# Performance work log

Measured on AMD Instinct MI355X. Metric: run time of the kernel, lower is better.

## Reference

```python
import jax, jax.numpy as jnp
import numpy as np

N_NODES = 50000
N_EDGES = 800000
D_FEAT = 128
UNITS = 128


def setup_inputs() -> dict:
    key = jax.random.key(0)
    k1, k2, k3, k4 = jax.random.split(key, 4)
    x = jax.random.normal(k1, (N_NODES, D_FEAT), dtype=jnp.float32)
    source = jax.random.randint(k2, (N_EDGES,), 0, N_NODES, dtype=jnp.int32)
    target = jax.random.randint(k3, (N_EDGES,), 0, N_NODES, dtype=jnp.int32)
    W = jax.random.normal(k4, (D_FEAT, UNITS), dtype=jnp.float32) * (1.0 / np.sqrt(D_FEAT))
    b = jnp.zeros((UNITS,), dtype=jnp.float32)
    return {"x": x, "source": source, "target": target, "W": W, "b": b}


def _degree(idx, n_nodes):
    # in/out degree = segment-sum of unit edge weights; clamp to >= 1 (no self loops)
    deg = jnp.zeros((n_nodes,), dtype=jnp.float32).at[idx].add(1.0)
    return jnp.maximum(deg, 1.0)


def reference(x, source, target, W, b):
    n = x.shape[0]
    # degree_normalization == "in_out": sender scale from out-degree, receiver from in-degree
    sender_scale = jax.lax.rsqrt(_degree(source, n))[:, None]      # [N, 1]
    receiver_scale = jax.lax.rsqrt(_degree(target, n))[:, None]    # [N, 1]
    normalized = sender_scale * x                                  # [N, D]
    source_bcast = normalized[source]                              # [E, D] gather
    pooled = jax.ops.segment_sum(source_bcast, target, num_segments=n)  # [N, D] scatter-add
    pooled = receiver_scale * pooled
    # Dense(units, activation='relu', use_bias=True)
    return jax.nn.relu(pooled @ W + b)
```

## Files before the change

kernel.cpp:

```cpp
#include <hip/hip_runtime.h>
#include <hip/hip_bf16.h>

#define N_FEAT 128
#define EPT 8
#define CHUNK 2048
#define BSHIFT 8
#define MAXRANGE 256
#define CAP 8192
#define LSTR 66

typedef short bf16x8 __attribute__((ext_vector_type(8)));
typedef float f32x4  __attribute__((ext_vector_type(4)));

__device__ __forceinline__ unsigned short f2bf_rtne(float f) {
    unsigned u = __float_as_uint(f);
    u += 0x7fffu + ((u >> 16) & 1u);
    return (unsigned short)(u >> 16);
}
__device__ __forceinline__ float bf2f(unsigned short h) {
    return __uint_as_float((unsigned)h << 16);
}

__global__ __launch_bounds__(256) void scatter_kernel(const int* __restrict__ source,
                                                      const int* __restrict__ target,
                                                      int* __restrict__ curT,
                                                      int* __restrict__ curS,
                                                      unsigned int* __restrict__ pairsT,
                                                      unsigned char* __restrict__ srcB,
                                                      const float* __restrict__ W,
                                                      unsigned short* __restrict__ Whi,
                                                      unsigned short* __restrict__ Wlo,
                                                      int E, int NB, int NBLK) {
    __shared__ unsigned int   lds_pairs[CHUNK];
    __shared__ unsigned short lds_sp[CHUNK];
    __shared__ int ct[MAXRANGE], cs[MAXRANGE];
    __shared__ int st[MAXRANGE], ss[MAXRANGE];
    __shared__ int gt[MAXRANGE], gs[MAXRANGE];
    int tid = threadIdx.x, b = blockIdx.x;

    if (b >= NBLK) {
        int idx = (b - NBLK) * 256 + tid;
        int lane = idx & 63;
        int ks = (idx >> 6) & 3;
        int ct2 = idx >> 8;
        int n  = ct2 * 16 + (lane & 15);
        int k0 = ks * 32 + (lane >> 4) * 8;
        unsigned short h[8], l[8];
        #pragma unroll
        for (int j = 0; j < 8; ++j) {
            float w = W[(k0 + j) * N_FEAT + n];
            unsigned short hh = f2bf_rtne(w);
            h[j] = hh;
            l[j] = f2bf_rtne(w - bf2f(hh));
        }
        size_t off = (size_t)idx * 8;
        *(ushort4*)(Whi + off)     = make_ushort4(h[0], h[1], h[2], h[3]);
        *(ushort4*)(Whi + off + 4) = make_ushort4(h[4], h[5], h[6], h[7]);
        *(ushort4*)(Wlo + off)     = make_ushort4(l[0], l[1], l[2], l[3]);
        *(ushort4*)(Wlo + off + 4) = make_ushort4(l[4], l[5], l[6], l[7]);
        return;
    }

    int base = b * CHUNK;
    int cnt = E - base; if (cnt > CHUNK) cnt = CHUNK;

    int rs[EPT], rt[EPT];
    ct[tid] = 0; cs[tid] = 0;
    __syncthreads();
    #pragma unroll
    for (int j = 0; j < EPT; ++j) {
        int e = base + j * 256 + tid;
        if (e < E) {
            int s = source[e], t = target[e];
            rs[j] = s; rt[j] = t;
            atomicAdd(&ct[t >> BSHIFT], 1);
            atomicAdd(&cs[s >> BSHIFT], 1);
        }
    }
    __syncthreads();
    int vt = ct[tid], vs = cs[tid];
    st[tid] = vt; ss[tid] = vs;
    __syncthreads();
    #pragma unroll
    for (int off = 1; off < 256; off <<= 1) {
        int t1 = (tid >= off) ? st[tid - off] : 0;
        int t2 = (tid >= off) ? ss[tid - off] : 0;
        __syncthreads();
        st[tid] += t1; ss[tid] += t2;
        __syncthreads();
    }
    int et = st[tid] - vt, es = ss[tid] - vs;
    int gT = 0, gS = 0;
    if (tid < NB) {
        if (vt) gT = atomicAdd(&curT[tid], vt);
        if (vs) gS = atomicAdd(&curS[tid], vs);
    }
    __syncthreads();
    st[tid] = et; ss[tid] = es;
    ct[tid] = et; cs[tid] = es;
    gt[tid] = gT; gs[tid] = gS;
    __syncthreads();
    #pragma unroll
    for (int j = 0; j < EPT; ++j) {
        int e = base + j * 256 + tid;
        if (e < E) {
            int s = rs[j], t = rt[j];
            int k = t >> BSHIFT;
            int p = atomicAdd(&ct[k], 1);
            lds_pairs[p] = (unsigned)s | ((unsigned)t << 16);
            int k2 = s >> BSHIFT;
            int p2 = atomicAdd(&cs[k2], 1);
            lds_sp[p2] = (unsigned short)s;
        }
    }
    __syncthreads();
    for (int i = tid; i < cnt; i += 256) {
        unsigned w = lds_pairs[i];
        int k = w >> 24;
        pairsT[(size_t)k * CAP + gt[k] + (i - st[k])] = w;
        unsigned short sp = lds_sp[i];
        int k2 = sp >> 8;
        srcB[(size_t)k2 * CAP + gs[k2] + (i - ss[k2])] = (unsigned char)sp;
    }
}

__global__ __launch_bounds__(256) void prep_kernel(const unsigned char* __restrict__ srcB,
                                                   const unsigned int* __restrict__ pairsT,
                                                   const int* __restrict__ curT,
                                                   const int* __restrict__ curS,
                                                   float* __restrict__ so,
                                                   int2* __restrict__ offs,
                                                   int* __restrict__ elist,
                                                   float* __restrict__ ri,
                                                   int N, int NB) {
    __shared__ int hist[MAXRANGE];
    __shared__ int sb[MAXRANGE];
    __shared__ int excl[MAXRANGE];
    __shared__ int cur[MAXRANGE];
    int tid = threadIdx.x, b = blockIdx.x;

    if (b < NB) {
        hist[tid] = 0;
        __syncthreads();
        int cnt = curS[b];
        size_t base = (size_t)b * CAP;
        for (int i = tid; i < cnt; i += 256)
            atomicAdd(&hist[srcB[base + i]], 1);
        __syncthreads();
        int node = (b << BSHIFT) + tid;
        if (node < N) {
            int d = hist[tid]; if (d < 1) d = 1;
            so[node] = rsqrtf((float)d);
        }
    } else {
        int bb = b - NB;
        hist[tid] = 0; cur[tid] = 0;
        __syncthreads();
        int cnt = curT[bb];
        int gbase = bb * CAP;
        for (int i = tid; i < cnt; i += 256)
            atomicAdd(&hist[(pairsT[(size_t)gbase + i] >> 16) & 255], 1);
        __syncthreads();
        int deg = hist[tid];
        sb[tid] = deg;
        __syncthreads();
        #pragma unroll
        for (int off = 1; off < 256; off <<= 1) {
            int t = (tid >= off) ? sb[tid - off] : 0;
            __syncthreads();
            sb[tid] += t;
            __syncthreads();
        }
        excl[tid] = sb[tid] - deg;
        __syncthreads();
        int node = (bb << BSHIFT) + tid;
        if (node < N) {
            int st0 = gbase + excl[tid];
            offs[node] = make_int2(st0, st0 + deg);
            int d = deg; if (d < 1) d = 1;
            ri[node] = rsqrtf((float)d);
        }
        for (int i = tid; i < cnt; i += 256) {
            unsigned w = pairsT[(size_t)gbase + i];
            int tl = (w >> 16) & 255;
            int pos = atomicAdd(&cur[tl], 1);
            elist[gbase + excl[tl] + pos] = (int)(w & 0xFFFFu);
        }
    }
}

__global__ __launch_bounds__(256) void ygemm_kernel(const float* __restrict__ x,
                                                    const float* __restrict__ so,
                                                    const unsigned short* __restrict__ Whi,
                                                    const unsigned short* __restrict__ Wlo,
                                                    unsigned short* __restrict__ Y,
                                                    int N) {
    __shared__ unsigned int hi_t[16 * LSTR];
    __shared__ unsigned int lo_t[16 * LSTR];
    int tid = threadIdx.x;
    int wave = tid >> 6, lane = tid & 63;
    int quad = lane >> 4, k16 = lane & 15;
    int row0 = blockIdx.x * 16;

    for (int i = tid; i < 1024; i += 256) {
        int r = i >> 6, dw = i & 63;
        int gr = row0 + r;
        float2 v = make_float2(0.f, 0.f);
        float s = 0.f;
        if (gr < N) {
            v = ((const float2*)x)[(size_t)gr * 64 + dw];
            s = so[gr];
        }
        float v0 = s * v.x, v1 = s * v.y;
        unsigned short h0 = f2bf_rtne(v0), h1 = f2bf_rtne(v1);
        unsigned short l0 = f2bf_rtne(v0 - bf2f(h0));
        unsigned short l1 = f2bf_rtne(v1 - bf2f(h1));
        hi_t[r * LSTR + dw] = (unsigned)h0 | ((unsigned)h1 << 16);
        lo_t[r * LSTR + dw] = (unsigned)l0 | ((unsigned)l1 << 16);
    }
    __syncthreads();

    bf16x8 Ahi[4], Alo[4];
    int m = k16;
    #pragma unroll
    for (int ks = 0; ks < 4; ++ks) {
        int a = m * LSTR + ks * 16 + quad * 4;
        Ahi[ks] = *(const bf16x8*)(hi_t + a);
        Alo[ks] = *(const bf16x8*)(lo_t + a);
    }
    const bf16x8* BH = (const bf16x8*)Whi;
    const bf16x8* BL = (const bf16x8*)Wlo;
    #pragma unroll
    for (int c = 0; c < 2; ++c) {
        int ctile = wave * 2 + c;
        f32x4 acc = {0.f, 0.f, 0.f, 0.f};
        #pragma unroll
        for (int ks = 0; ks < 4; ++ks) {
            bf16x8 bh = BH[(ctile * 4 + ks) * 64 + lane];
            bf16x8 bl = BL[(ctile * 4 + ks) * 64 + lane];
            acc = __builtin_amdgcn_mfma_f32_16x16x32_bf16(Ahi[ks], bh, acc, 0, 0, 0);
            acc = __builtin_amdgcn_mfma_f32_16x16x32_bf16(Alo[ks], bh, acc, 0, 0, 0);
            acc = __builtin_amdgcn_mfma_f32_16x16x32_bf16(Ahi[ks], bl, acc, 0, 0, 0);
        }
        int colc = ctile * 16 + m;
        #pragma unroll
        for (int reg = 0; reg < 4; ++reg) {
            int gr = row0 + quad * 4 + reg;
            if (gr < N)
                Y[(size_t)gr * N_FEAT + colc] = f2bf_rtne(acc[reg]);
        }
    }
}

#define ACC8(u) { acc[0] += __uint_as_float((u).x << 16); \
                  acc[1] += __uint_as_float((u).x & 0xffff0000u); \
                  acc[2] += __uint_as_float((u).y << 16); \
                  acc[3] += __uint_as_float((u).y & 0xffff0000u); \
                  acc[4] += __uint_as_float((u).z << 16); \
                  acc[5] += __uint_as_float((u).z & 0xffff0000u); \
                  acc[6] += __uint_as_float((u).w << 16); \
                  acc[7] += __uint_as_float((u).w & 0xffff0000u); }

__global__ __launch_bounds__(128) void agg_kernel(const unsigned short* __restrict__ Y,
                                                  const int* __restrict__ elist,
                                                  const int2* __restrict__ offs,
                                                  const float* __restrict__ ri,
                                                  const float* __restrict__ bias,
                                                  float* __restrict__ out,
                                                  int N) {
    int tid  = threadIdx.x;
    int wave = tid >> 6, lane = tid & 63;
    int quad = lane >> 4, k16 = lane & 15;
    int node = blockIdx.x * 8 + wave * 4 + quad;
    if (node >= N) return;
    const uint4* yr = (const uint4*)Y;
    int2 oe = offs[node];
    float rr = ri[node];
    float acc[8] = {0.f, 0.f, 0.f, 0.f, 0.f, 0.f, 0.f, 0.f};
    int j = oe.x, je = oe.y;
    for (; j + 8 <= je; j += 8) {
        int e0 = elist[j],     e1 = elist[j + 1];
        int e2 = elist[j + 2], e3 = elist[j + 3];
        int e4 = elist[j + 4], e5 = elist[j + 5];
        int e6 = elist[j + 6], e7 = elist[j + 7];
        uint4 u0 = yr[(size_t)e0 * 16 + k16];
        uint4 u1 = yr[(size_t)e1 * 16 + k16];
        uint4 u2 = yr[(size_t)e2 * 16 + k16];
        uint4 u3 = yr[(size_t)e3 * 16 + k16];
        uint4 u4 = yr[(size_t)e4 * 16 + k16];
        uint4 u5 = yr[(size_t)e5 * 16 + k16];
        uint4 u6 = yr[(size_t)e6 * 16 + k16];
        uint4 u7 = yr[(size_t)e7 * 16 + k16];
        ACC8(u0) ACC8(u1) ACC8(u2) ACC8(u3)
        ACC8(u4) ACC8(u5) ACC8(u6) ACC8(u7)
    }
    for (; j < je; ++j) {
        int e = elist[j];
        uint4 u = yr[(size_t)e * 16 + k16];
        ACC8(u)
    }
    int f0 = k16 * 8;
    const float4* bp = (const float4*)(bias + f0);
    float4 b0 = bp[0], b1 = bp[1];
    float4 o0, o1;
    o0.x = fmaxf(acc[0] * rr + b0.x, 0.f);
    o0.y = fmaxf(acc[1] * rr + b0.y, 0.f);
    o0.z = fmaxf(acc[2] * rr + b0.z, 0.f);
    o0.w = fmaxf(acc[3] * rr + b0.w, 0.f);
    o1.x = fmaxf(acc[4] * rr + b1.x, 0.f);
    o1.y = fmaxf(acc[5] * rr + b1.y, 0.f);
    o1.z = fmaxf(acc[6] * rr + b1.z, 0.f);
    o1.w = fmaxf(acc[7] * rr + b1.w, 0.f);
    float4* op = (float4*)(out + (size_t)node * N_FEAT + f0);
    op[0] = o0;
    op[1] = o1;
}

extern "C" void kernel_launch(void* const* d_in, const int* in_sizes, int n_in,
                              void* d_out, int out_size, void* d_ws, size_t ws_size,
                              hipStream_t stream) {
    const float* x      = (const float*)d_in[0];
    const int*   source = (const int*)d_in[1];
    const int*   target = (const int*)d_in[2];
    const float* W      = (const float*)d_in[3];
    const float* bias   = (const float*)d_in[4];
    float*       out    = (float*)d_out;

    const int N = in_sizes[0] / N_FEAT;
    const int E = in_sizes[1];

    const int NB   = (N + MAXRANGE - 1) >> BSHIFT;
    const int NBLK = (E + CHUNK - 1) / CHUNK;

    uintptr_t p = (uintptr_t)d_ws;
    auto carve = [&](size_t bytes) {
        p = (p + 255) & ~(uintptr_t)255;
        uintptr_t r = p;
        p += bytes;
        return (void*)r;
    };
    int*            curs    = (int*)carve((size_t)2 * NB * sizeof(int));
    int*            curT    = curs;
    int*            curS    = curs + NB;
    unsigned int*   pairsT  = (unsigned int*)carve((size_t)NB * CAP * sizeof(unsigned int));
    int*            elist   = (int*)carve((size_t)NB * CAP * sizeof(int));
    unsigned char*  srcB    = (unsigned char*)carve((size_t)NB * CAP);
    float*          ri      = (float*)carve((size_t)N * sizeof(float));
    float*          so      = (float*)carve((size_t)N * sizeof(float));
    int2*           offs    = (int2*)carve((size_t)N * sizeof(int2));
    unsigned short* Y       = (unsigned short*)carve((size_t)N * N_FEAT * sizeof(unsigned short));
    unsigned short* Whi     = (unsigned short*)carve((size_t)N_FEAT * N_FEAT * sizeof(unsigned short));
    unsigned short* Wlo     = (unsigned short*)carve((size_t)N_FEAT * N_FEAT * sizeof(unsigned short));
    (void)ws_size; (void)n_in; (void)out_size;

    (void)hipMemsetAsync(curs, 0, (size_t)2 * NB * sizeof(int), stream);

    scatter_kernel<<<NBLK + 8, 256, 0, stream>>>(source, target, curT, curS, pairsT, srcB,
                                                 W, Whi, Wlo, E, NB, NBLK);
    prep_kernel<<<2 * NB, 256, 0, stream>>>(srcB, pairsT, curT, curS, so,
                                            offs, elist, ri, N, NB);
    ygemm_kernel<<<(N + 15) / 16, 256, 0, stream>>>(x, so, Whi, Wlo, Y, N);
    agg_kernel<<<(N + 7) / 8, 128, 0, stream>>>(Y, elist, offs, ri, bias, out, N);
}
```

Before: 159.1 us.

## Fuse out-degree and GEMM into prep kernel, use wave-shuffle scans, halve chunk

The separate Y=(so*x)@W GEMM kernel is folded into prep_kernel as extra blocks. Each GEMM block now computes the out-degree of its own 16 rows by scanning that bucket's srcB bytes, so the separate so array and one kernel launch are gone. The LDS-based 256-wide prefix scans are replaced with wave shuffle scans plus a small cross-wave combine, and the scatter chunk is halved to 1024 edges per block. The cost is that every GEMM block redundantly rescans a whole source bucket (about 16 blocks share each bucket), and the scatter kernel now needs twice as many blocks and twice as many global atomics.

```diff
diff --git a/kernel.cpp b/kernel.cpp
--- a/kernel.cpp
+++ b/kernel.cpp
@@ -2,8 +2,8 @@
 #include <hip/hip_bf16.h>
 
 #define N_FEAT 128
-#define EPT 8
-#define CHUNK 2048
+#define EPT 4
+#define CHUNK 1024
 #define BSHIFT 8
 #define MAXRANGE 256
 #define CAP 8192
@@ -36,15 +36,17 @@
     __shared__ int ct[MAXRANGE], cs[MAXRANGE];
     __shared__ int st[MAXRANGE], ss[MAXRANGE];
     __shared__ int gt[MAXRANGE], gs[MAXRANGE];
+    __shared__ int wsT[4], wsS[4];
     int tid = threadIdx.x, b = blockIdx.x;
+    int wave = tid >> 6, lane = tid & 63;
 
     if (b >= NBLK) {
         int idx = (b - NBLK) * 256 + tid;
-        int lane = idx & 63;
+        int ln = idx & 63;
         int ks = (idx >> 6) & 3;
         int ct2 = idx >> 8;
-        int n  = ct2 * 16 + (lane & 15);
-        int k0 = ks * 32 + (lane >> 4) * 8;
+        int n  = ct2 * 16 + (ln & 15);
+        int k0 = ks * 32 + (ln >> 4) * 8;
         unsigned short h[8], l[8];
         #pragma unroll
         for (int j = 0; j < 8; ++j) {
@@ -79,23 +81,24 @@
     }
     __syncthreads();
     int vt = ct[tid], vs = cs[tid];
-    st[tid] = vt; ss[tid] = vs;
-    __syncthreads();
+    int it = vt, is = vs;
     #pragma unroll
-    for (int off = 1; off < 256; off <<= 1) {
-        int t1 = (tid >= off) ? st[tid - off] : 0;
-        int t2 = (tid >= off) ? ss[tid - off] : 0;
-        __syncthreads();
-        st[tid] += t1; ss[tid] += t2;
-        __syncthreads();
-    }
-    int et = st[tid] - vt, es = ss[tid] - vs;
+    for (int off = 1; off < 64; off <<= 1) {
+        int a = __shfl_up(it, off);
+        int c = __shfl_up(is, off);
+        if (lane >= off) { it += a; is += c; }
+    }
+    if (lane == 63) { wsT[wave] = it; wsS[wave] = is; }
+    __syncthreads();
+    int bT = 0, bS = 0;
+    for (int w2 = 0; w2 < wave; ++w2) { bT += wsT[w2]; bS += wsS[w2]; }
+    it += bT; is += bS;
+    int et = it - vt, es = is - vs;
     int gT = 0, gS = 0;
     if (tid < NB) {
         if (vt) gT = atomicAdd(&curT[tid], vt);
         if (vs) gS = atomicAdd(&curS[tid], vs);
     }
-    __syncthreads();
     st[tid] = et; ss[tid] = es;
     ct[tid] = et; cs[tid] = es;
     gt[tid] = gT; gs[tid] = gS;
@@ -128,32 +131,28 @@
                                                    const unsigned int* __restrict__ pairsT,
                                                    const int* __restrict__ curT,
                                                    const int* __restrict__ curS,
-                                                   float* __restrict__ so,
+                                                   const float* __restrict__ x,
+                                                   const unsigned short* __restrict__ Whi,
+                                                   const unsigned short* __restrict__ Wlo,
+                                                   unsigned short* __restrict__ Y,
                                                    int2* __restrict__ offs,
                                                    int* __restrict__ elist,
                                                    float* __restrict__ ri,
                                                    int N, int NB) {
     __shared__ int hist[MAXRANGE];
-    __shared__ int sb[MAXRANGE];
     __shared__ int excl[MAXRANGE];
     __shared__ int cur[MAXRANGE];
+    __shared__ int ws[4];
+    __shared__ int h16[16];
+    __shared__ float so16[16];
+    __shared__ unsigned int hi_t[16 * LSTR];
+    __shared__ unsigned int lo_t[16 * LSTR];
     int tid = threadIdx.x, b = blockIdx.x;
+    int wave = tid >> 6, lane = tid & 63;
+    int quad = lane >> 4, k16 = lane & 15;
 
     if (b < NB) {
-        hist[tid] = 0;
-        __syncthreads();
-        int cnt = curS[b];
-        size_t base = (size_t)b * CAP;
-        for (int i = tid; i < cnt; i += 256)
-            atomicAdd(&hist[srcB[base + i]], 1);
-        __syncthreads();
-        int node = (b << BSHIFT) + tid;
-        if (node < N) {
-            int d = hist[tid]; if (d < 1) d = 1;
-            so[node] = rsqrtf((float)d);
-        }
-    } else {
-        int bb = b - NB;
+        int bb = b;
         hist[tid] = 0; cur[tid] = 0;
         __syncthreads();
         int cnt = curT[bb];
@@ -162,16 +161,18 @@
             atomicAdd(&hist[(pairsT[(size_t)gbase + i] >> 16) & 255], 1);
         __syncthreads();
         int deg = hist[tid];
-        sb[tid] = deg;
-        __syncthreads();
+        int v = deg;
         #pragma unroll
-        for (int off = 1; off < 256; off <<= 1) {
-            int t = (tid >= off) ? sb[tid - off] : 0;
-            __syncthreads();
-            sb[tid] += t;
-            __syncthreads();
-        }
-        excl[tid] = sb[tid] - deg;
+        for (int off = 1; off < 64; off <<= 1) {
+            int a = __shfl_up(v, off);
+            if (lane >= off) v += a;
+        }
+        if (lane == 63) ws[wave] = v;
+        __syncthreads();
+        int bsum = 0;
+        for (int w2 = 0; w2 < wave; ++w2) bsum += ws[w2];
+        v += bsum;
+        excl[tid] = v - deg;
         __syncthreads();
         int node = (bb << BSHIFT) + tid;
         if (node < N) {
@@ -186,68 +187,83 @@
             int pos = atomicAdd(&cur[tl], 1);
             elist[gbase + excl[tl] + pos] = (int)(w & 0xFFFFu);
         }
-    }
-}
-
-__global__ __launch_bounds__(256) void ygemm_kernel(const float* __restrict__ x,
-                                                    const float* __restrict__ so,
-                                                    const unsigned short* __restrict__ Whi,
-                                                    const unsigned short* __restrict__ Wlo,
-                                                    unsigned short* __restrict__ Y,
-                                                    int N) {
-    __shared__ unsigned int hi_t[16 * LSTR];
-    __shared__ unsigned int lo_t[16 * LSTR];
-    int tid = threadIdx.x;
-    int wave = tid >> 6, lane = tid & 63;
-    int quad = lane >> 4, k16 = lane & 15;
-    int row0 = blockIdx.x * 16;
-
-    for (int i = tid; i < 1024; i += 256) {
-        int r = i >> 6, dw = i & 63;
-        int gr = row0 + r;
-        float2 v = make_float2(0.f, 0.f);
-        float s = 0.f;
-        if (gr < N) {
-            v = ((const float2*)x)[(size_t)gr * 64 + dw];
-            s = so[gr];
-        }
-        float v0 = s * v.x, v1 = s * v.y;
-        unsigned short h0 = f2bf_rtne(v0), h1 = f2bf_rtne(v1);
-        unsigned short l0 = f2bf_rtne(v0 - bf2f(h0));
-        unsigned short l1 = f2bf_rtne(v1 - bf2f(h1));
-        hi_t[r * LSTR + dw] = (unsigned)h0 | ((unsigned)h1 << 16);
-        lo_t[r * LSTR + dw] = (unsigned)l0 | ((unsigned)l1 << 16);
-    }
-    __syncthreads();
-
-    bf16x8 Ahi[4], Alo[4];
-    int m = k16;
-    #pragma unroll
-    for (int ks = 0; ks < 4; ++ks) {
-        int a = m * LSTR + ks * 16 + quad * 4;
-        Ahi[ks] = *(const bf16x8*)(hi_t + a);
-        Alo[ks] = *(const bf16x8*)(lo_t + a);
-    }
-    const bf16x8* BH = (const bf16x8*)Whi;
-    const bf16x8* BL = (const bf16x8*)Wlo;
-    #pragma unroll
-    for (int c = 0; c < 2; ++c) {
-        int ctile = wave * 2 + c;
-        f32x4 acc = {0.f, 0.f, 0.f, 0.f};
+    } else {
+        int row0 = (b - NB) * 16;
+        int bb2 = row0 >> BSHIFT;
+        int lo = row0 & 255;
+        if (tid < 16) h16[tid] = 0;
+        __syncthreads();
+        int scnt = curS[bb2];
+        const uint4* sp4 = (const uint4*)(srcB + (size_t)bb2 * CAP);
+        int nvec = (scnt + 15) >> 4;
+        for (int i4 = tid; i4 < nvec; i4 += 256) {
+            uint4 u = sp4[i4];
+            unsigned wd[4] = { u.x, u.y, u.z, u.w };
+            #pragma unroll
+            for (int w2 = 0; w2 < 4; ++w2) {
+                #pragma unroll
+                for (int bj = 0; bj < 4; ++bj) {
+                    int g = i4 * 16 + w2 * 4 + bj;
+                    if (g < scnt) {
+                        unsigned d = (wd[w2] >> (8 * bj)) & 255u;
+                        unsigned r = d - (unsigned)lo;
+                        if (r < 16u) atomicAdd(&h16[r], 1);
+                    }
+                }
+            }
+        }
+        __syncthreads();
+        if (tid < 16) {
+            int d = h16[tid]; if (d < 1) d = 1;
+            so16[tid] = rsqrtf((float)d);
+        }
+        __syncthreads();
+        for (int i = tid; i < 1024; i += 256) {
+            int r = i >> 6, dw = i & 63;
+            int gr = row0 + r;
+            float2 vv = make_float2(0.f, 0.f);
+            float s = 0.f;
+            if (gr < N) {
+                vv = ((const float2*)x)[(size_t)gr * 64 + dw];
+                s = so16[r];
+            }
+            float v0 = s * vv.x, v1 = s * vv.y;
+            unsigned short h0 = f2bf_rtne(v0), h1 = f2bf_rtne(v1);
+            unsigned short l0 = f2bf_rtne(v0 - bf2f(h0));
+            unsigned short l1 = f2bf_rtne(v1 - bf2f(h1));
+            hi_t[r * LSTR + dw] = (unsigned)h0 | ((unsigned)h1 << 16);
+            lo_t[r * LSTR + dw] = (unsigned)l0 | ((unsigned)l1 << 16);
+        }
+        __syncthreads();
+        bf16x8 Ahi[4], Alo[4];
+        int m = k16;
         #pragma unroll
         for (int ks = 0; ks < 4; ++ks) {
-            bf16x8 bh = BH[(ctile * 4 + ks) * 64 + lane];
-            bf16x8 bl = BL[(ctile * 4 + ks) * 64 + lane];
-            acc = __builtin_amdgcn_mfma_f32_16x16x32_bf16(Ahi[ks], bh, acc, 0, 0, 0);
-            acc = __builtin_amdgcn_mfma_f32_16x16x32_bf16(Alo[ks], bh, acc, 0, 0, 0);
-            acc = __builtin_amdgcn_mfma_f32_16x16x32_bf16(Ahi[ks], bl, acc, 0, 0, 0);
-        }
-        int colc = ctile * 16 + m;
+            int a = m * LSTR + ks * 16 + quad * 4;
+            Ahi[ks] = *(const bf16x8*)(hi_t + a);
+            Alo[ks] = *(const bf16x8*)(lo_t + a);
+        }
+        const bf16x8* BH = (const bf16x8*)Whi;
+        const bf16x8* BL = (const bf16x8*)Wlo;
         #pragma unroll
-        for (int reg = 0; reg < 4; ++reg) {
-            int gr = row0 + quad * 4 + reg;
-            if (gr < N)
-                Y[(size_t)gr * N_FEAT + colc] = f2bf_rtne(acc[reg]);
+        for (int c = 0; c < 2; ++c) {
+            int ctile = wave * 2 + c;
+            f32x4 acc = {0.f, 0.f, 0.f, 0.f};
+            #pragma unroll
+            for (int ks = 0; ks < 4; ++ks) {
+                bf16x8 bh = BH[(ctile * 4 + ks) * 64 + lane];
+                bf16x8 bl = BL[(ctile * 4 + ks) * 64 + lane];
+                acc = __builtin_amdgcn_mfma_f32_16x16x32_bf16(Ahi[ks], bh, acc, 0, 0, 0);
+                acc = __builtin_amdgcn_mfma_f32_16x16x32_bf16(Alo[ks], bh, acc, 0, 0, 0);
+                acc = __builtin_amdgcn_mfma_f32_16x16x32_bf16(Ahi[ks], bl, acc, 0, 0, 0);
+            }
+            int colc = ctile * 16 + m;
+            #pragma unroll
+            for (int reg = 0; reg < 4; ++reg) {
+                int gr = row0 + quad * 4 + reg;
+                if (gr < N)
+                    Y[(size_t)gr * N_FEAT + colc] = f2bf_rtne(acc[reg]);
+            }
         }
     }
 }
@@ -346,7 +362,6 @@
     int*            elist   = (int*)carve((size_t)NB * CAP * sizeof(int));
     unsigned char*  srcB    = (unsigned char*)carve((size_t)NB * CAP);
     float*          ri      = (float*)carve((size_t)N * sizeof(float));
-    float*          so      = (float*)carve((size_t)N * sizeof(float));
     int2*           offs    = (int2*)carve((size_t)N * sizeof(int2));
     unsigned short* Y       = (unsigned short*)carve((size_t)N * N_FEAT * sizeof(unsigned short));
     unsigned short* Whi     = (unsigned short*)carve((size_t)N_FEAT * N_FEAT * sizeof(unsigned short));
@@ -357,8 +372,7 @@
 
     scatter_kernel<<<NBLK + 8, 256, 0, stream>>>(source, target, curT, curS, pairsT, srcB,
                                                  W, Whi, Wlo, E, NB, NBLK);
-    prep_kernel<<<2 * NB, 256, 0, stream>>>(srcB, pairsT, curT, curS, so,
-                                            offs, elist, ri, N, NB);
-    ygemm_kernel<<<(N + 15) / 16, 256, 0, stream>>>(x, so, Whi, Wlo, Y, N);
+    prep_kernel<<<NB + (N + 15) / 16, 256, 0, stream>>>(srcB, pairsT, curT, curS, x,
+                                                        Whi, Wlo, Y, offs, elist, ri, N, NB);
     agg_kernel<<<(N + 7) / 8, 128, 0, stream>>>(Y, elist, offs, ri, bias, out, N);
 }
```

Result: no change. 159.5 us (+0.2%).
